# Kernel optimization log

Hardware: AMD Instinct MI355X
Metric: run time of the kernel (lower is better)

The kernel has to match this reference:

```python
import jax, jax.numpy as jnp
import numpy as np

R_MAX = 32
S_MAX = 2
C_Z = 128
IN_DIM = 4 * R_MAX + 2 * S_MAX + 7  # 139
N = 1024


def setup_inputs() -> dict:
    key = jax.random.key(0)
    k1, k2, k3, k4, k5, k6 = jax.random.split(key, 6)
    return {
        "asym_id": jax.random.randint(k1, (N,), 0, 8, dtype=jnp.int64 if jax.config.jax_enable_x64 else jnp.int32),
        "residue_index": jax.random.randint(k2, (N,), 0, 512),
        "entity_id": jax.random.randint(k3, (N,), 0, 4),
        "token_index": jax.random.randint(k4, (N,), 0, 2048),
        "sym_id": jax.random.randint(k5, (N,), 0, 4),
        "weight": jax.random.normal(k6, (C_Z, IN_DIM), dtype=jnp.float32),
    }


def reference(asym_id, residue_index, entity_id, token_index, sym_id, weight):
    r_max, s_max = R_MAX, S_MAX
    pos_dim = 2 * r_max + 2    # 66
    token_dim = 2 * r_max + 2  # 66
    # Pre-projected one-hot rows -> lookup tables (original casts to fp16, accumulates fp32)
    w16 = weight.astype(jnp.float16)
    W_pos = w16[:, :pos_dim].T                                # [66, c_z]
    W_token = w16[:, pos_dim:pos_dim + token_dim].T            # [66, c_z]
    W_entity = w16[:, pos_dim + token_dim]                     # [c_z]
    W_chain = w16[:, pos_dim + token_dim + 1:].T               # [6, c_z]

    same_chain = asym_id[:, None] == asym_id[None, :]          # [N, N]
    same_res = residue_index[:, None] == residue_index[None, :]
    same_ent = entity_id[:, None] == entity_id[None, :]

    d_res = jnp.clip(residue_index[:, None] - residue_index[None, :] + r_max, 0, 2 * r_max)
    d_res = jnp.where(same_chain, d_res, 2 * r_max + 1)

    d_tok = jnp.clip(token_index[:, None] - token_index[None, :] + r_max, 0, 2 * r_max)
    d_tok = jnp.where(same_chain & same_res, d_tok, 2 * r_max + 1)

    d_ch = jnp.clip(sym_id[:, None] - sym_id[None, :] + s_max, 0, 2 * s_max)
    d_ch = jnp.where(same_ent, d_ch, 2 * s_max + 1)

    out = (
        W_pos[d_res].astype(jnp.float32)
        + W_token[d_tok].astype(jnp.float32)
        + W_chain[d_ch].astype(jnp.float32)
        + jnp.where(same_ent[:, :, None], W_entity.astype(jnp.float32)[None, None, :], 0.0)
    )  # [N, N, c_z] fp32
    return out
```

## Files before the change

### kernel.cpp

```cpp
#include <hip/hip_runtime.h>
#include <hip/hip_fp16.h>

constexpr int NN    = 1024;
constexpr int CZ    = 128;
constexpr int INDIM = 139;

typedef float f4 __attribute__((ext_vector_type(4)));

constexpr int TBL_FLOATS = 18432;
constexpr int TBL_BYTES  = TBL_FLOATS * 4;

__global__ void build_tables(const int* __restrict__ asym, const int* __restrict__ resi,
                             const int* __restrict__ ent,  const int* __restrict__ tok,
                             const int* __restrict__ sym,  const float* __restrict__ w,
                             float* __restrict__ tbl, unsigned* __restrict__ packed)
{
    const int gtid   = blockIdx.x * 256 + threadIdx.x;
    const int stride = gridDim.x * 256;

    for (int idx = gtid; idx < 8448; idx += stride) {
        const int d = idx >> 7, c = idx & 127;
        tbl[idx]        = __half2float(__float2half(w[c * INDIM + d]));
        tbl[8448 + idx] = __half2float(__float2half(w[c * INDIM + 66 + d]));
    }
    for (int idx = gtid; idx < 768; idx += stride) {
        const int d = idx >> 7, c = idx & 127;
        const float ch = __half2float(__float2half(w[c * INDIM + 133 + d]));
        const float en = __half2float(__float2half(w[c * INDIM + 132]));
        tbl[16896 + idx]       = ch;
        tbl[16896 + 768 + idx] = ch + en;
    }
    for (int j = gtid; j < NN; j += stride) {
        packed[j] = (unsigned)(asym[j] & 7)
                  | ((unsigned)(ent[j]  & 3)    << 3)
                  | ((unsigned)(sym[j]  & 3)    << 5)
                  | ((unsigned)(resi[j] & 1023) << 7)
                  | ((unsigned)(tok[j]  & 4095) << 17);
    }
}

__global__ __launch_bounds__(256, 2) void relpos_main(
    const float* __restrict__ tbl, const unsigned* __restrict__ packed,
    float* __restrict__ out)
{
    __shared__ __attribute__((aligned(16))) float    lds[TBL_FLOATS];
    __shared__ __attribute__((aligned(16))) unsigned attrs[NN];

    const int tid = threadIdx.x;

    {
        const f4* __restrict__ src = (const f4*)tbl;
        f4* __restrict__ dst = (f4*)lds;
        #pragma unroll
        for (int k = 0; k < 18; ++k) dst[tid + 256 * k] = src[tid + 256 * k];
    }
    #pragma unroll
    for (int k = 0; k < 4; ++k) attrs[tid + 256 * k] = packed[tid + 256 * k];
    __syncthreads();

    const int i0 = blockIdx.x << 1;

    const unsigned pi0 = packed[i0];
    const unsigned pi1 = packed[i0 + 1];
    const int a0 = pi0 & 7, e0 = (pi0 >> 3) & 3, s0 = (pi0 >> 5) & 3;
    const int r0 = (pi0 >> 7) & 1023, t0 = (pi0 >> 17) & 4095;
    const int a1 = pi1 & 7, e1 = (pi1 >> 3) & 3, s1 = (pi1 >> 5) & 3;
    const int r1 = (pi1 >> 7) & 1023, t1 = (pi1 >> 17) & 4095;

    const int g  = tid >> 5;
    const int c4 = (tid & 31) << 2;

    float* outp0 = out + ((size_t)i0 << 17) + (size_t)g * CZ + c4;
    float* outp1 = outp0 + (1 << 17);

    #pragma unroll 4
    for (int jt = 0; jt < 128; ++jt) {
        const unsigned pj = attrs[jt * 8 + g];
        const int aj = pj & 7, ej = (pj >> 3) & 3, sj = (pj >> 5) & 3;
        const int rj = (pj >> 7) & 1023, tj = (pj >> 17) & 4095;

        {
            const bool sc = (a0 == aj);
            const bool sr = (r0 == rj);
            const int  se = (e0 == ej) ? 1 : 0;
            int dres = min(max(r0 - rj + 32, 0), 64);
            if (!sc) dres = 65;
            int dtok = min(max(t0 - tj + 32, 0), 64);
            if (!(sc && sr)) dtok = 65;
            int dch = min(max(s0 - sj + 2, 0), 4);
            if (!se) dch = 5;

            const f4 p  = *(const f4*)&lds[dres * 128 + c4];
            const f4 t  = *(const f4*)&lds[8448 + dtok * 128 + c4];
            const f4 cc = *(const f4*)&lds[16896 + se * 768 + dch * 128 + c4];
            __builtin_nontemporal_store(p + t + cc, (f4*)outp0);
        }
        {
            const bool sc = (a1 == aj);
            const bool sr = (r1 == rj);
            const int  se = (e1 == ej) ? 1 : 0;
            int dres = min(max(r1 - rj + 32, 0), 64);
            if (!sc) dres = 65;
            int dtok = min(max(t1 - tj + 32, 0), 64);
            if (!(sc && sr)) dtok = 65;
            int dch = min(max(s1 - sj + 2, 0), 4);
            if (!se) dch = 5;

            const f4 p  = *(const f4*)&lds[dres * 128 + c4];
            const f4 t  = *(const f4*)&lds[8448 + dtok * 128 + c4];
            const f4 cc = *(const f4*)&lds[16896 + se * 768 + dch * 128 + c4];
            __builtin_nontemporal_store(p + t + cc, (f4*)outp1);
        }
        outp0 += 8 * CZ;
        outp1 += 8 * CZ;
    }
}

extern "C" void kernel_launch(void* const* d_in, const int* in_sizes, int n_in,
                              void* d_out, int out_size, void* d_ws, size_t ws_size,
                              hipStream_t stream) {
    const int*   asym   = (const int*)d_in[0];
    const int*   resi   = (const int*)d_in[1];
    const int*   ent    = (const int*)d_in[2];
    const int*   tok    = (const int*)d_in[3];
    const int*   sym    = (const int*)d_in[4];
    const float* weight = (const float*)d_in[5];
    float*       out    = (float*)d_out;

    float*    tbl    = (float*)d_ws;
    unsigned* packed = (unsigned*)((char*)d_ws + TBL_BYTES);

    build_tables<<<16, 256, 0, stream>>>(asym, resi, ent, tok, sym, weight, tbl, packed);
    relpos_main<<<NN / 2, 256, 0, stream>>>(tbl, packed, out);
}
```

Measured before the change: 540.4 us.

## Fuse table construction into main kernel, building fp16-rounded tables in LDS per block

Removes the separate build_tables launch and its global workspace. Each block now loads the raw weight matrix into LDS, packs the per-token attributes itself, transposes and fp16-rounds the tables through registers (72 per thread), and writes them back to LDS. This removes a kernel launch and the dependency between the two kernels. In exchange every one of the 512 blocks repeats the table build, which adds extra syncs and register pressure to a kernel that is bound by output bandwidth.

```diff
diff --git a/kernel.cpp b/kernel.cpp
--- a/kernel.cpp
+++ b/kernel.cpp
@@ -4,43 +4,21 @@
 constexpr int NN    = 1024;
 constexpr int CZ    = 128;
 constexpr int INDIM = 139;
+constexpr int RAWW  = INDIM * CZ;
 
 typedef float f4 __attribute__((ext_vector_type(4)));
 
 constexpr int TBL_FLOATS = 18432;
-constexpr int TBL_BYTES  = TBL_FLOATS * 4;
+constexpr int KPT        = TBL_FLOATS / 256;
 
-__global__ void build_tables(const int* __restrict__ asym, const int* __restrict__ resi,
-                             const int* __restrict__ ent,  const int* __restrict__ tok,
-                             const int* __restrict__ sym,  const float* __restrict__ w,
-                             float* __restrict__ tbl, unsigned* __restrict__ packed)
-{
-    const int gtid   = blockIdx.x * 256 + threadIdx.x;
-    const int stride = gridDim.x * 256;
-
-    for (int idx = gtid; idx < 8448; idx += stride) {
-        const int d = idx >> 7, c = idx & 127;
-        tbl[idx]        = __half2float(__float2half(w[c * INDIM + d]));
-        tbl[8448 + idx] = __half2float(__float2half(w[c * INDIM + 66 + d]));
-    }
-    for (int idx = gtid; idx < 768; idx += stride) {
-        const int d = idx >> 7, c = idx & 127;
-        const float ch = __half2float(__float2half(w[c * INDIM + 133 + d]));
-        const float en = __half2float(__float2half(w[c * INDIM + 132]));
-        tbl[16896 + idx]       = ch;
-        tbl[16896 + 768 + idx] = ch + en;
-    }
-    for (int j = gtid; j < NN; j += stride) {
-        packed[j] = (unsigned)(asym[j] & 7)
-                  | ((unsigned)(ent[j]  & 3)    << 3)
-                  | ((unsigned)(sym[j]  & 3)    << 5)
-                  | ((unsigned)(resi[j] & 1023) << 7)
-                  | ((unsigned)(tok[j]  & 4095) << 17);
-    }
+__device__ __forceinline__ float q16(float x) {
+    return __half2float(__float2half(x));
 }
 
-__global__ __launch_bounds__(256, 2) void relpos_main(
-    const float* __restrict__ tbl, const unsigned* __restrict__ packed,
+__global__ __launch_bounds__(256, 2) void relpos_fused(
+    const int* __restrict__ asym, const int* __restrict__ resi,
+    const int* __restrict__ ent,  const int* __restrict__ tok,
+    const int* __restrict__ sym,  const float* __restrict__ w,
     float* __restrict__ out)
 {
     __shared__ __attribute__((aligned(16))) float    lds[TBL_FLOATS];
@@ -48,20 +26,48 @@
 
     const int tid = threadIdx.x;
 
-    {
-        const f4* __restrict__ src = (const f4*)tbl;
-        f4* __restrict__ dst = (f4*)lds;
-        #pragma unroll
-        for (int k = 0; k < 18; ++k) dst[tid + 256 * k] = src[tid + 256 * k];
+    for (int k = tid; k < RAWW; k += 256) lds[k] = w[k];
+    #pragma unroll
+    for (int k = 0; k < 4; ++k) {
+        const int j = tid + 256 * k;
+        attrs[j] = (unsigned)(asym[j] & 7)
+                 | ((unsigned)(ent[j]  & 3)    << 3)
+                 | ((unsigned)(sym[j]  & 3)    << 5)
+                 | ((unsigned)(resi[j] & 1023) << 7)
+                 | ((unsigned)(tok[j]  & 4095) << 17);
     }
+    __syncthreads();
+
+    float r[KPT];
     #pragma unroll
-    for (int k = 0; k < 4; ++k) attrs[tid + 256 * k] = packed[tid + 256 * k];
+    for (int k = 0; k < KPT; ++k) {
+        const int idx = tid + 256 * k;
+        if (k < 33) {
+            const int d = idx >> 7, c = idx & 127;
+            r[k] = q16(lds[c * INDIM + d]);
+        } else if (k < 66) {
+            const int i2 = idx - 8448;
+            const int d = i2 >> 7, c = i2 & 127;
+            r[k] = q16(lds[c * INDIM + 66 + d]);
+        } else {
+            const int i3  = idx - 16896;
+            const int se  = (k >= 69) ? 1 : 0;
+            const int rem = i3 - se * 768;
+            const int d = rem >> 7, c = rem & 127;
+            float v = q16(lds[c * INDIM + 133 + d]);
+            if (se) v += q16(lds[c * INDIM + 132]);
+            r[k] = v;
+        }
+    }
+    __syncthreads();
+
+    #pragma unroll
+    for (int k = 0; k < KPT; ++k) lds[tid + 256 * k] = r[k];
     __syncthreads();
 
     const int i0 = blockIdx.x << 1;
-
-    const unsigned pi0 = packed[i0];
-    const unsigned pi1 = packed[i0 + 1];
+    const unsigned pi0 = attrs[i0];
+    const unsigned pi1 = attrs[i0 + 1];
     const int a0 = pi0 & 7, e0 = (pi0 >> 3) & 3, s0 = (pi0 >> 5) & 3;
     const int r0 = (pi0 >> 7) & 1023, t0 = (pi0 >> 17) & 4095;
     const int a1 = pi1 & 7, e1 = (pi1 >> 3) & 3, s1 = (pi1 >> 5) & 3;
@@ -127,9 +133,5 @@
     const float* weight = (const float*)d_in[5];
     float*       out    = (float*)d_out;
 
-    float*    tbl    = (float*)d_ws;
-    unsigned* packed = (unsigned*)((char*)d_ws + TBL_BYTES);
-
-    build_tables<<<16, 256, 0, stream>>>(asym, resi, ent, tok, sym, weight, tbl, packed);
-    relpos_main<<<NN / 2, 256, 0, stream>>>(tbl, packed, out);
+    relpos_fused<<<NN / 2, 256, 0, stream>>>(asym, resi, ent, tok, sym, weight, out);
 }
```

Result: no change. 538.9 us (-0.3%).
